# Kernel optimization log

Hardware: AMD Instinct MI355X
Metric: run time of the kernel (lower is better)

The kernel has to match this reference:

```python
import jax, jax.numpy as jnp
import numpy as np

BS, DIM, N_CLASSES = 4096, 512, 100
POS_W, NEG_W = 2.0, 40.0
MARGIN, POS_T, NEG_T = 0.1, 0.5, 0.5


def setup_inputs() -> dict:
    key = jax.random.key(0)
    k1, k2 = jax.random.split(key)
    x = jax.random.normal(k1, (BS, DIM), dtype=jnp.float32)
    x = x / jnp.linalg.norm(x, axis=-1, keepdims=True)  # cosine-mode embeddings
    labels = jax.random.randint(k2, (BS,), 0, N_CLASSES, dtype=jnp.int64 if jax.config.jax_enable_x64 else jnp.int32)
    return {"batch": x, "labels": labels}


def _masked_logsumexp(sims, mask, use_max):
    # Faithful port of Criterion.masked_logsumexp with dim=0 (per-column).
    m = sims * mask  # bool mask promotes; masked-out entries become 0
    ref = jnp.max(m, axis=0) if use_max else jnp.min(m, axis=0)  # (BS,)
    ref = jax.lax.stop_gradient(ref)
    nz = (jnp.max(m, axis=0) + jnp.min(m, axis=0)) != 0  # columns with any nonzero masked entry
    s = jnp.sum(jnp.exp(sims - ref[None, :]) * mask, axis=0)  # (BS,)
    vals = jnp.log(jnp.where(nz, s, 1.0)) + ref
    return vals, nz


def _masked_mean_softplus(vals, nz, w):
    cnt = jnp.sum(nz).astype(vals.dtype)
    sp = jax.nn.softplus(vals) / w
    mean = jnp.sum(jnp.where(nz, sp, 0.0)) / jnp.maximum(cnt, 1.0)
    # torch path returns scalar 0 from masked_logsumexp when no nz columns -> softplus(0)/w
    return jnp.where(cnt > 0, mean, jax.nn.softplus(0.0) / w)


def reference(batch, labels):
    sim = batch @ batch.T                                  # (BS, BS) cosine similarity
    same = labels[:, None] == labels[None, :]
    diff = ~same
    eye = jnp.eye(sim.shape[0], dtype=bool)

    # per-row bounds: hardest positive (min sim, excl. self) / hardest negative (max sim)
    pos_bound = jnp.min(jnp.where(same & ~eye, sim, jnp.inf), axis=1)   # (BS,)
    neg_bound = jnp.max(jnp.where(diff, sim, -jnp.inf), axis=1)        # (BS,)

    # torch broadcasting applies bounds per-COLUMN (last dim)
    neg_mask = diff & (sim + MARGIN > pos_bound[None, :])
    pos_mask = same & (sim - MARGIN < neg_bound[None, :])

    w_pos = -POS_W * (sim - POS_T)
    w_neg = NEG_W * (sim - NEG_T)

    pos_vals, pos_nz = _masked_logsumexp(w_pos, pos_mask, use_max=False)
    neg_vals, neg_nz = _masked_logsumexp(w_neg, neg_mask, use_max=True)

    loss = _masked_mean_softplus(pos_vals, pos_nz, POS_W) \
         + _masked_mean_softplus(neg_vals, neg_nz, NEG_W)
    return loss
```

## Files before the change

### kernel.cpp

```cpp
#include <hip/hip_runtime.h>
#include <stdint.h>


#define BS 4096
#define DIM 512
#define NTILES 528
#define NSLOT 32

typedef __attribute__((ext_vector_type(8))) short short8;
typedef __attribute__((ext_vector_type(4))) float f32x4;

#define TILE_USH (128 * 64)

#define VMW0 asm volatile("s_waitcnt vmcnt(0)" ::: "memory")

__device__ __forceinline__ ushort f2bf(float f){
  unsigned u = __float_as_uint(f);
  return (ushort)((u + 0x7fffu + ((u >> 16) & 1u)) >> 16);
}
__device__ __forceinline__ void gld_lds16(void* ldsp, const void* gp){
  __builtin_amdgcn_global_load_lds((const __attribute__((address_space(1))) void*)gp,
                                   (__attribute__((address_space(3))) void*)ldsp, 16, 0, 0);
}

__global__ void k_convert(const float* __restrict__ x, ushort* __restrict__ xh){
  int i = blockIdx.x * blockDim.x + threadIdx.x;
  float4 v = ((const float4*)x)[i];
  ((ushort4*)xh)[i] = make_ushort4(f2bf(v.x), f2bf(v.y), f2bf(v.z), f2bf(v.w));
}

__device__ __forceinline__ void decode_tile(int bid, int& Rm, int& Rn, bool& diag){
  int wg = (bid & 7) * 66 + (bid >> 3);
  int ii = wg, bm = 0;
  while (ii >= 32 - bm){ ii -= 32 - bm; ++bm; }
  const int bn = bm + ii;
  diag = (bm == bn);
  Rm = bm * 128; Rn = bn * 128;
}

__device__ __forceinline__ void stage_ks(ushort* dstA, ushort* dstB,
                                         const ushort* __restrict__ Xh,
                                         int Rm, int Rn, int ks,
                                         int r0, int gx, int lds_i){
  const int kb = ks * 64 + gx * 8;
  #pragma unroll
  for (int rep = 0; rep < 4; ++rep){
    const int row = rep * 32 + r0;
    const int lo  = rep * 2048 + lds_i;
    gld_lds16(dstA + lo, Xh + (size_t)(Rm + row) * DIM + kb);
    gld_lds16(dstB + lo, Xh + (size_t)(Rn + row) * DIM + kb);
  }
}

__device__ __forceinline__ void gemm_tile_db(f32x4 (&acc)[4][4],
                                             ushort (&lds)[2][2 * TILE_USH],
                                             const ushort* __restrict__ Xh,
                                             int Rm, int Rn, int t)
{
  const int l  = t & 63;
  const int w  = t >> 6;
  const int wm = w >> 1, wn = w & 1;
  const int lc = l & 15;
  const int lq = l >> 4;
  const int r0 = t >> 3;
  const int gx = (t & 7) ^ (r0 & 7);
  const int lds_i = t * 8;

  #pragma unroll
  for (int i = 0; i < 4; ++i)
    #pragma unroll
    for (int j = 0; j < 4; ++j) acc[i][j] = (f32x4){0.f, 0.f, 0.f, 0.f};

  stage_ks(&lds[0][0], &lds[0][TILE_USH], Xh, Rm, Rn, 0, r0, gx, lds_i);
  VMW0;
  __builtin_amdgcn_s_barrier();
  __builtin_amdgcn_sched_barrier(0);

  #pragma unroll
  for (int ks = 0; ks < 8; ++ks){
    const int cur = ks & 1;
    if (ks < 7)
      stage_ks(&lds[cur ^ 1][0], &lds[cur ^ 1][TILE_USH], Xh, Rm, Rn, ks + 1, r0, gx, lds_i);
    #pragma unroll
    for (int kk = 0; kk < 2; ++kk){
      const int gr = kk * 4 + lq;
      const int sl = (gr ^ (l & 7)) * 8;
      short8 ah[4], bh[4];
      #pragma unroll
      for (int f = 0; f < 4; ++f){
        ah[f] = *(const short8*)&lds[cur][(wm * 64 + f * 16 + lc) * 64 + sl];
        bh[f] = *(const short8*)&lds[cur][TILE_USH + (wn * 64 + f * 16 + lc) * 64 + sl];
      }
      #pragma unroll
      for (int fm = 0; fm < 4; ++fm)
        #pragma unroll
        for (int fn = 0; fn < 4; ++fn)
          acc[fm][fn] = __builtin_amdgcn_mfma_f32_16x16x32_bf16(ah[fm], bh[fn], acc[fm][fn], 0, 0, 0);
    }
    __builtin_amdgcn_sched_barrier(0);
    VMW0;
    __builtin_amdgcn_s_barrier();
    __builtin_amdgcn_sched_barrier(0);
  }
}

__global__ __launch_bounds__(256)
void k_bounds(const ushort* __restrict__ Xh, const int* __restrict__ labels,
              float* __restrict__ posB, float* __restrict__ negB)
{
  __shared__ ushort lds[2][2 * TILE_USH];
  const int t = threadIdx.x;
  int Rm, Rn; bool diag;
  decode_tile((int)blockIdx.x, Rm, Rn, diag);
  const int bm = Rm >> 7, bn = Rn >> 7;

  f32x4 acc[4][4];
  gemm_tile_db(acc, lds, Xh, Rm, Rn, t);

  const int l  = t & 63;
  const int w  = t >> 6;
  const int wm = w >> 1, wn = w & 1;
  const int lc = l & 15, lq = l >> 4;
  const float INF = __builtin_inff();

  int labr[4][4];
  #pragma unroll
  for (int fm = 0; fm < 4; ++fm)
    #pragma unroll
    for (int v = 0; v < 4; ++v)
      labr[fm][v] = labels[Rm + wm * 64 + fm * 16 + lq * 4 + v];

  __syncthreads();
  float* sMnS = (float*)&lds[0][0];
  float* sMxS = sMnS + 256;
  float* sMnT = sMnS + 512;
  float* sMxT = sMnS + 768;

  #pragma unroll
  for (int fm = 0; fm < 4; ++fm){
    float mn[4] = {INF, INF, INF, INF};
    float mx[4] = {-INF, -INF, -INF, -INF};
    #pragma unroll
    for (int fn = 0; fn < 4; ++fn){
      const int gc = Rn + wn * 64 + fn * 16 + lc;
      const int labc = labels[gc];
      #pragma unroll
      for (int v = 0; v < 4; ++v){
        const float s = acc[fm][fn][v];
        const int grow = Rm + wm * 64 + fm * 16 + lq * 4 + v;
        const bool same = (labc == labr[fm][v]);
        mn[v] = fminf(mn[v], (same && (grow != gc)) ? s : INF);
        mx[v] = fmaxf(mx[v], same ? -INF : s);
      }
    }
    #pragma unroll
    for (int off = 1; off < 16; off <<= 1)
      #pragma unroll
      for (int v = 0; v < 4; ++v){
        mn[v] = fminf(mn[v], __shfl_xor(mn[v], off));
        mx[v] = fmaxf(mx[v], __shfl_xor(mx[v], off));
      }
    if (lc == 0){
      #pragma unroll
      for (int v = 0; v < 4; ++v){
        const int r64 = fm * 16 + lq * 4 + v;
        sMnS[(wm * 2 + wn) * 64 + r64] = mn[v];
        sMxS[(wm * 2 + wn) * 64 + r64] = mx[v];
      }
    }
  }
  if (!diag){
    #pragma unroll
    for (int fn = 0; fn < 4; ++fn){
      const int gc = Rn + wn * 64 + fn * 16 + lc;
      const int labc = labels[gc];
      float mn = INF, mx = -INF;
      #pragma unroll
      for (int fm = 0; fm < 4; ++fm)
        #pragma unroll
        for (int v = 0; v < 4; ++v){
          const float s = acc[fm][fn][v];
          const bool same = (labc == labr[fm][v]);
          mn = fminf(mn, same ? s : INF);
          mx = fmaxf(mx, same ? -INF : s);
        }
      #pragma unroll
      for (int off = 16; off < 64; off <<= 1){
        mn = fminf(mn, __shfl_xor(mn, off));
        mx = fmaxf(mx, __shfl_xor(mx, off));
      }
      if (l < 16){
        const int c64 = fn * 16 + lc;
        sMnT[(wn * 2 + wm) * 64 + c64] = mn;
        sMxT[(wn * 2 + wm) * 64 + c64] = mx;
      }
    }
  }
  __syncthreads();
  if (t < 128){
    const int h = t >> 6, r = t & 63;
    posB[(size_t)bn * BS + Rm + t] = fminf(sMnS[(h * 2 + 0) * 64 + r], sMnS[(h * 2 + 1) * 64 + r]);
    negB[(size_t)bn * BS + Rm + t] = fmaxf(sMxS[(h * 2 + 0) * 64 + r], sMxS[(h * 2 + 1) * 64 + r]);
    if (!diag){
      posB[(size_t)bm * BS + Rn + t] = fminf(sMnT[(h * 2 + 0) * 64 + r], sMnT[(h * 2 + 1) * 64 + r]);
      negB[(size_t)bm * BS + Rn + t] = fmaxf(sMxT[(h * 2 + 0) * 64 + r], sMxT[(h * 2 + 1) * 64 + r]);
    }
  }
}

__global__ void k_redbounds(const float* __restrict__ posB, const float* __restrict__ negB,
                            float* __restrict__ pos_bound, float* __restrict__ neg_bound){
  const int r = blockIdx.x * 256 + threadIdx.x;
  float mn = __builtin_inff(), mx = -__builtin_inff();
  #pragma unroll
  for (int s = 0; s < NSLOT; ++s){
    mn = fminf(mn, posB[(size_t)s * BS + r]);
    mx = fmaxf(mx, negB[(size_t)s * BS + r]);
  }
  pos_bound[r] = mn;
  neg_bound[r] = mx;
}

__global__ __launch_bounds__(256)
void k_stats(const ushort* __restrict__ Xh, const int* __restrict__ labels,
             const float* __restrict__ pos_bound, const float* __restrict__ neg_bound,
             float* __restrict__ SNp, float* __restrict__ SPp)
{
  __shared__ ushort lds[2][2 * TILE_USH];
  const int t = threadIdx.x;
  int Rm, Rn; bool diag;
  decode_tile((int)blockIdx.x, Rm, Rn, diag);
  const int bm = Rm >> 7, bn = Rn >> 7;

  f32x4 acc[4][4];
  gemm_tile_db(acc, lds, Xh, Rm, Rn, t);

  const int l  = t & 63;
  const int w  = t >> 6;
  const int wm = w >> 1, wn = w & 1;
  const int lc = l & 15, lq = l >> 4;

  int labr[4][4];
  #pragma unroll
  for (int fm = 0; fm < 4; ++fm)
    #pragma unroll
    for (int v = 0; v < 4; ++v)
      labr[fm][v] = labels[Rm + wm * 64 + fm * 16 + lq * 4 + v];

  __syncthreads();
  float* sSNs = (float*)&lds[0][0];
  float* sSPs = sSNs + 256;
  float* sSNt = sSNs + 512;
  float* sSPt = sSNs + 768;

  #pragma unroll
  for (int fn = 0; fn < 4; ++fn){
    const int gc = Rn + wn * 64 + fn * 16 + lc;
    const int labc = labels[gc];
    const float pb = pos_bound[gc];
    const float nb = neg_bound[gc];
    float sN = 0.f, sP = 0.f;
    #pragma unroll
    for (int fm = 0; fm < 4; ++fm)
      #pragma unroll
      for (int v = 0; v < 4; ++v){
        const float s = acc[fm][fn][v];
        const bool same = (labc == labr[fm][v]);
        sN += ((!same) && (s + 0.1f > pb)) ? __expf(40.0f * (s - 0.5f)) : 0.0f;
        sP += (same && (s - 0.1f < nb))    ? __expf(-2.0f * (s - 0.5f)) : 0.0f;
      }
    #pragma unroll
    for (int off = 16; off < 64; off <<= 1){
      sN += __shfl_xor(sN, off);
      sP += __shfl_xor(sP, off);
    }
    if (l < 16){
      const int c64 = fn * 16 + lc;
      sSNs[(wn * 2 + wm) * 64 + c64] = sN;
      sSPs[(wn * 2 + wm) * 64 + c64] = sP;
    }
  }
  if (!diag){
    #pragma unroll
    for (int fm = 0; fm < 4; ++fm){
      float pbr[4], nbr[4];
      #pragma unroll
      for (int v = 0; v < 4; ++v){
        const int grow = Rm + wm * 64 + fm * 16 + lq * 4 + v;
        pbr[v] = pos_bound[grow];
        nbr[v] = neg_bound[grow];
      }
      float sN[4] = {0.f, 0.f, 0.f, 0.f}, sP[4] = {0.f, 0.f, 0.f, 0.f};
      #pragma unroll
      for (int fn = 0; fn < 4; ++fn){
        const int gc = Rn + wn * 64 + fn * 16 + lc;
        const int labc = labels[gc];
        #pragma unroll
        for (int v = 0; v < 4; ++v){
          const float s = acc[fm][fn][v];
          const bool same = (labc == labr[fm][v]);
          sN[v] += ((!same) && (s + 0.1f > pbr[v])) ? __expf(40.0f * (s - 0.5f)) : 0.0f;
          sP[v] += (same && (s - 0.1f < nbr[v]))    ? __expf(-2.0f * (s - 0.5f)) : 0.0f;
        }
      }
      #pragma unroll
      for (int off = 1; off < 16; off <<= 1)
        #pragma unroll
        for (int v = 0; v < 4; ++v){
          sN[v] += __shfl_xor(sN[v], off);
          sP[v] += __shfl_xor(sP[v], off);
        }
      if (lc == 0){
        #pragma unroll
        for (int v = 0; v < 4; ++v){
          const int r64 = fm * 16 + lq * 4 + v;
          sSNt[(wm * 2 + wn) * 64 + r64] = sN[v];
          sSPt[(wm * 2 + wn) * 64 + r64] = sP[v];
        }
      }
    }
  }
  __syncthreads();
  if (t < 128){
    const int h = t >> 6, r = t & 63;
    SNp[(size_t)bm * BS + Rn + t] = sSNs[(h * 2 + 0) * 64 + r] + sSNs[(h * 2 + 1) * 64 + r];
    SPp[(size_t)bm * BS + Rn + t] = sSPs[(h * 2 + 0) * 64 + r] + sSPs[(h * 2 + 1) * 64 + r];
    if (!diag){
      SNp[(size_t)bn * BS + Rm + t] = sSNt[(h * 2 + 0) * 64 + r] + sSNt[(h * 2 + 1) * 64 + r];
      SPp[(size_t)bn * BS + Rm + t] = sSPt[(h * 2 + 0) * 64 + r] + sSPt[(h * 2 + 1) * 64 + r];
    }
  }
}

__global__ void k_redstats(const float* __restrict__ SNp, const float* __restrict__ SPp,
                           float4* __restrict__ part)
{
  const int t = threadIdx.x;
  const int c = blockIdx.x * 256 + t;
  float sn = 0.f, sp = 0.f;
  #pragma unroll
  for (int s = 0; s < NSLOT; ++s){
    sn += SNp[(size_t)s * BS + c];
    sp += SPp[(size_t)s * BS + c];
  }
  float sumP = (sp != 0.f) ? log1pf(sp) : 0.f;
  float cP   = (sp != 0.f) ? 1.f : 0.f;
  float sumN = (sn != 0.f) ? log1pf(sn) : 0.f;
  float cN   = (sn != 0.f) ? 1.f : 0.f;
  #pragma unroll
  for (int off = 32; off; off >>= 1){
    sumP += __shfl_down(sumP, off); cP += __shfl_down(cP, off);
    sumN += __shfl_down(sumN, off); cN += __shfl_down(cN, off);
  }
  __shared__ float red[4][4];
  const int w = t >> 6;
  if ((t & 63) == 0){ red[w][0] = sumP; red[w][1] = cP; red[w][2] = sumN; red[w][3] = cN; }
  __syncthreads();
  if (t == 0){
    float a = 0.f, b = 0.f, c2 = 0.f, d = 0.f;
    for (int i = 0; i < 4; ++i){ a += red[i][0]; b += red[i][1]; c2 += red[i][2]; d += red[i][3]; }
    part[blockIdx.x] = make_float4(a, b, c2, d);
  }
}

__global__ void k_final2(const float4* __restrict__ part, float* __restrict__ out)
{
  const int l = threadIdx.x;
  float4 v = (l < 16) ? part[l] : make_float4(0.f, 0.f, 0.f, 0.f);
  float sumP = v.x, cP = v.y, sumN = v.z, cN = v.w;
  #pragma unroll
  for (int off = 8; off; off >>= 1){
    sumP += __shfl_down(sumP, off); cP += __shfl_down(cP, off);
    sumN += __shfl_down(sumN, off); cN += __shfl_down(cN, off);
  }
  if (l == 0){
    const float LN2 = 0.69314718055994531f;
    const float tP = (cP > 0.f) ? (sumP / 2.0f)  / fmaxf(cP, 1.f) : LN2 / 2.0f;
    const float tN = (cN > 0.f) ? (sumN / 40.0f) / fmaxf(cN, 1.f) : LN2 / 40.0f;
    out[0] = tP + tN;
  }
}

extern "C" void kernel_launch(void* const* d_in, const int* in_sizes, int n_in,
                              void* d_out, int out_size, void* d_ws, size_t ws_size,
                              hipStream_t stream) {
  const float* x    = (const float*)d_in[0];
  const int* labels = (const int*)d_in[1];
  char* W = (char*)d_ws;
  ushort* Xh        = (ushort*)W;
  float*  P1        = (float*)(W + (4u << 20));
  float*  P2        = (float*)(W + (4u << 20) + (512u << 10));
  float*  pos_bound = (float*)(W + (5u << 20));
  float*  neg_bound = (float*)(W + (5u << 20) + (16u << 10));
  float4* part      = (float4*)(W + (5u << 20) + (32u << 10));

  k_convert<<<(BS * DIM / 4) / 256, 256, 0, stream>>>(x, Xh);
  k_bounds<<<NTILES, 256, 0, stream>>>(Xh, labels, P1, P2);
  k_redbounds<<<BS / 256, 256, 0, stream>>>(P1, P2, pos_bound, neg_bound);
  k_stats<<<NTILES, 256, 0, stream>>>(Xh, labels, pos_bound, neg_bound, P1, P2);
  k_redstats<<<BS / 256, 256, 0, stream>>>(P1, P2, part);
  k_final2<<<1, 64, 0, stream>>>(part, (float*)d_out);
}
```

Before: 151.6 us.

## Replace double-buffered K loop with 4-stage BK=32 LDS pipeline

```diff
diff --git a/kernel.cpp b/kernel.cpp
--- a/kernel.cpp
+++ b/kernel.cpp
@@ -6,13 +6,13 @@
 #define DIM 512
 #define NTILES 528
 #define NSLOT 32
+#define NK 16
+#define BK 32
+#define BUF_USH 8192
+#define PANEL_USH 4096
 
 typedef __attribute__((ext_vector_type(8))) short short8;
 typedef __attribute__((ext_vector_type(4))) float f32x4;
-
-#define TILE_USH (128 * 64)
-
-#define VMW0 asm volatile("s_waitcnt vmcnt(0)" ::: "memory")
 
 __device__ __forceinline__ ushort f2bf(float f){
   unsigned u = __float_as_uint(f);
@@ -38,68 +38,65 @@
   Rm = bm * 128; Rn = bn * 128;
 }
 
-__device__ __forceinline__ void stage_ks(ushort* dstA, ushort* dstB,
-                                         const ushort* __restrict__ Xh,
-                                         int Rm, int Rn, int ks,
-                                         int r0, int gx, int lds_i){
-  const int kb = ks * 64 + gx * 8;
-  #pragma unroll
-  for (int rep = 0; rep < 4; ++rep){
-    const int row = rep * 32 + r0;
-    const int lo  = rep * 2048 + lds_i;
-    gld_lds16(dstA + lo, Xh + (size_t)(Rm + row) * DIM + kb);
-    gld_lds16(dstB + lo, Xh + (size_t)(Rn + row) * DIM + kb);
-  }
-}
-
-__device__ __forceinline__ void gemm_tile_db(f32x4 (&acc)[4][4],
-                                             ushort (&lds)[2][2 * TILE_USH],
-                                             const ushort* __restrict__ Xh,
-                                             int Rm, int Rn, int t)
+__device__ __forceinline__ void stage_ks(ushort* buf,
+                                         const ushort* __restrict__ gA,
+                                         const ushort* __restrict__ gB,
+                                         int ks, int t){
+  const int gx = (t & 3) ^ ((t >> 2) & 3);
+  const int kb = ks * BK + gx * 8;
+  #pragma unroll
+  for (int rep = 0; rep < 2; ++rep){
+    const int row = rep * 64 + (t >> 2);
+    const int lo  = (rep * 256 + t) * 8;
+    gld_lds16(buf + lo,             gA + (size_t)row * DIM + kb);
+    gld_lds16(buf + PANEL_USH + lo, gB + (size_t)row * DIM + kb);
+  }
+}
+
+__device__ __forceinline__ void gemm_tile_pipe(f32x4 (&acc)[4][4],
+                                               ushort (&lds)[4][BUF_USH],
+                                               const ushort* __restrict__ Xh,
+                                               int Rm, int Rn, int t)
 {
   const int l  = t & 63;
   const int w  = t >> 6;
   const int wm = w >> 1, wn = w & 1;
   const int lc = l & 15;
   const int lq = l >> 4;
-  const int r0 = t >> 3;
-  const int gx = (t & 7) ^ (r0 & 7);
-  const int lds_i = t * 8;
+  const ushort* gA = Xh + (size_t)Rm * DIM;
+  const ushort* gB = Xh + (size_t)Rn * DIM;
 
   #pragma unroll
   for (int i = 0; i < 4; ++i)
     #pragma unroll
     for (int j = 0; j < 4; ++j) acc[i][j] = (f32x4){0.f, 0.f, 0.f, 0.f};
 
-  stage_ks(&lds[0][0], &lds[0][TILE_USH], Xh, Rm, Rn, 0, r0, gx, lds_i);
-  VMW0;
-  __builtin_amdgcn_s_barrier();
-  __builtin_amdgcn_sched_barrier(0);
-
-  #pragma unroll
-  for (int ks = 0; ks < 8; ++ks){
-    const int cur = ks & 1;
-    if (ks < 7)
-      stage_ks(&lds[cur ^ 1][0], &lds[cur ^ 1][TILE_USH], Xh, Rm, Rn, ks + 1, r0, gx, lds_i);
-    #pragma unroll
-    for (int kk = 0; kk < 2; ++kk){
-      const int gr = kk * 4 + lq;
-      const int sl = (gr ^ (l & 7)) * 8;
-      short8 ah[4], bh[4];
-      #pragma unroll
-      for (int f = 0; f < 4; ++f){
-        ah[f] = *(const short8*)&lds[cur][(wm * 64 + f * 16 + lc) * 64 + sl];
-        bh[f] = *(const short8*)&lds[cur][TILE_USH + (wn * 64 + f * 16 + lc) * 64 + sl];
-      }
-      #pragma unroll
-      for (int fm = 0; fm < 4; ++fm)
-        #pragma unroll
-        for (int fn = 0; fn < 4; ++fn)
-          acc[fm][fn] = __builtin_amdgcn_mfma_f32_16x16x32_bf16(ah[fm], bh[fn], acc[fm][fn], 0, 0, 0);
-    }
+  stage_ks(&lds[0][0], gA, gB, 0, t);
+  stage_ks(&lds[1][0], gA, gB, 1, t);
+  stage_ks(&lds[2][0], gA, gB, 2, t);
+
+  #pragma unroll
+  for (int ks = 0; ks < NK; ++ks){
+    if (ks < NK - 2)      asm volatile("s_waitcnt vmcnt(8)" ::: "memory");
+    else if (ks == NK-2)  asm volatile("s_waitcnt vmcnt(4)" ::: "memory");
+    else                  asm volatile("s_waitcnt vmcnt(0)" ::: "memory");
+    __builtin_amdgcn_s_barrier();
     __builtin_amdgcn_sched_barrier(0);
-    VMW0;
-    __builtin_amdgcn_s_barrier();
+    if (ks + 3 < NK)
+      stage_ks(&lds[(ks + 3) & 3][0], gA, gB, ks + 3, t);
+    const ushort* buf = &lds[ks & 3][0];
+    const int sl = (lq ^ (lc & 3)) * 8;
+    short8 ah[4], bh[4];
+    #pragma unroll
+    for (int f = 0; f < 4; ++f){
+      ah[f] = *(const short8*)&buf[(wm * 64 + f * 16 + lc) * BK + sl];
+      bh[f] = *(const short8*)&buf[PANEL_USH + (wn * 64 + f * 16 + lc) * BK + sl];
+    }
+    #pragma unroll
+    for (int fm = 0; fm < 4; ++fm)
+      #pragma unroll
+      for (int fn = 0; fn < 4; ++fn)
+        acc[fm][fn] = __builtin_amdgcn_mfma_f32_16x16x32_bf16(ah[fm], bh[fn], acc[fm][fn], 0, 0, 0);
     __builtin_amdgcn_sched_barrier(0);
   }
 }
@@ -108,14 +105,14 @@
 void k_bounds(const ushort* __restrict__ Xh, const int* __restrict__ labels,
               float* __restrict__ posB, float* __restrict__ negB)
 {
-  __shared__ ushort lds[2][2 * TILE_USH];
+  __shared__ ushort lds[4][BUF_USH];
   const int t = threadIdx.x;
   int Rm, Rn; bool diag;
   decode_tile((int)blockIdx.x, Rm, Rn, diag);
   const int bm = Rm >> 7, bn = Rn >> 7;
 
   f32x4 acc[4][4];
-  gemm_tile_db(acc, lds, Xh, Rm, Rn, t);
+  gemm_tile_pipe(acc, lds, Xh, Rm, Rn, t);
 
   const int l  = t & 63;
   const int w  = t >> 6;
@@ -226,14 +223,14 @@
              const float* __restrict__ pos_bound, const float* __restrict__ neg_bound,
              float* __restrict__ SNp, float* __restrict__ SPp)
 {
-  __shared__ ushort lds[2][2 * TILE_USH];
+  __shared__ ushort lds[4][BUF_USH];
   const int t = threadIdx.x;
   int Rm, Rn; bool diag;
   decode_tile((int)blockIdx.x, Rm, Rn, diag);
   const int bm = Rm >> 7, bn = Rn >> 7;
 
   f32x4 acc[4][4];
-  gemm_tile_db(acc, lds, Xh, Rm, Rn, t);
+  gemm_tile_pipe(acc, lds, Xh, Rm, Rn, t);
 
   const int l  = t & 63;
   const int w  = t >> 6;
```

Result: no change. 154.4 us (+1.8%).
